# Kernel tuning notes

Measured on AMD Instinct MI355X. Metric: run time of the kernel, lower is better.

The kernel has to match this reference:

```python
import jax, jax.numpy as jnp
import numpy as np

B, T, D_IN, D_H, D_OUT = 64, 1024, 128, 512, 128


def setup_inputs() -> dict:
    key = jax.random.key(0)
    k1, k2, k3, k4, k5 = jax.random.split(key, 5)
    hscale = 0.1
    ifactor = 1.0 / np.sqrt(D_IN)
    hfactor = 1.0 / np.sqrt(D_H)
    pfactor = 1.0 / np.sqrt(D_H)
    return {
        "input_seq": jax.random.normal(k1, (B, T, D_IN), dtype=jnp.float32),
        "h0": jax.random.normal(k2, (D_H,), dtype=jnp.float32) * hscale,
        "wI": jax.random.normal(k3, (D_IN, D_H), dtype=jnp.float32) * ifactor,
        "wR": jax.random.normal(k4, (D_H, D_H), dtype=jnp.float32) * hfactor,
        "wO": jax.random.normal(k5, (D_H, D_OUT), dtype=jnp.float32) * pfactor,
    }


def reference(input_seq, h0, wI, wR, wO):
    # Precompute input projections for all timesteps at once: (B, T, D_H)
    xI = jnp.einsum("bti,ih->bth", input_seq, wI)
    h_init = jnp.broadcast_to(h0, (input_seq.shape[0], h0.shape[0]))

    def step(h, xI_t):
        h = jnp.tanh(xI_t + h @ wR)  # (B, D_H)
        return h, h

    # scan over time axis: move T to leading axis
    _, H = jax.lax.scan(step, h_init, jnp.swapaxes(xI, 0, 1))
    H = jnp.swapaxes(H, 0, 1)  # (B, T, D_H)
    O = jnp.einsum("bth,ho->bto", H, wO)  # (B, T, D_OUT)
    return O, H
```

## Files before the change

kernel.cpp:

```cpp
#include <hip/hip_runtime.h>
#include <cstdint>
#include <cstddef>

typedef _Float16 f16;
typedef _Float16 f16x4 __attribute__((ext_vector_type(4)));
typedef _Float16 f16x8 __attribute__((ext_vector_type(8)));
typedef float f32x4 __attribute__((ext_vector_type(4)));

#define MFMA16(a, b, c) __builtin_amdgcn_mfma_f32_16x16x16f16((a), (b), (c), 0, 0, 0)
#define MFMA32(a, b, c) __builtin_amdgcn_mfma_f32_16x16x32_f16((a), (b), (c), 0, 0, 0)

constexpr int TT = 1024, DIN = 128, DH = 512, DOUT = 128;
constexpr size_t O_ELEMS = (size_t)64 * 1024 * 128;

__device__ __forceinline__ uint32_t SW(uint32_t r) {
    return ((r & 7u) << 4) ^ ((r & 8u) << 2);
}

__global__ __launch_bounds__(256, 1) void k_xI(const float* __restrict__ X,
                                               const float* __restrict__ wI,
                                               float* __restrict__ xI) {
    __shared__ __align__(16) f16 Bt[DH][136];
    __shared__ __align__(16) f16 At[64][136];
    const int tid = threadIdx.x;
    const int wv = tid >> 6, ln = tid & 63, l15 = ln & 15, g = ln >> 4;
    const int m0 = (int)blockIdx.x * 64;

    #pragma unroll
    for (int u = 0; u < 16; ++u) {
        const int uid = u * 256 + tid;
        const int c4 = (uid & 127) << 2;
        const int r4 = (uid >> 7) << 2;
        float4 w[4];
        #pragma unroll
        for (int j = 0; j < 4; ++j)
            w[j] = *(const float4*)(wI + (size_t)(r4 + j) * DH + c4);
        #pragma unroll
        for (int n = 0; n < 4; ++n) {
            f16x4 v;
            #pragma unroll
            for (int j = 0; j < 4; ++j) v[j] = (f16)((&w[j].x)[n]);
            *(f16x4*)(&Bt[c4 + n][r4]) = v;
        }
    }
    {
        int r = tid >> 2;
        int cb = (tid & 3) << 5;
        #pragma unroll
        for (int u = 0; u < 8; ++u) {
            int c = cb + u * 4;
            const float4 x4 = *(const float4*)(X + (size_t)(m0 + r) * DIN + c);
            f16x4 h4;
            h4[0] = (f16)x4.x; h4[1] = (f16)x4.y; h4[2] = (f16)x4.z; h4[3] = (f16)x4.w;
            *(f16x4*)((char*)&At[r][0] + c * 2) = h4;
        }
    }
    __syncthreads();

    f32x4 acc[4][8];
    #pragma unroll
    for (int mt = 0; mt < 4; ++mt)
        #pragma unroll
        for (int nt = 0; nt < 8; ++nt) acc[mt][nt] = (f32x4){0.f, 0.f, 0.f, 0.f};

    #pragma unroll
    for (int c = 0; c < 8; ++c) {
        const int k0 = c * 16 + g * 4;
        f16x4 a[4];
        #pragma unroll
        for (int mt = 0; mt < 4; ++mt)
            a[mt] = *(const f16x4*)((const char*)&At[mt * 16 + l15][0] + k0 * 2);
        #pragma unroll
        for (int nt = 0; nt < 8; ++nt) {
            const int n = wv * 128 + nt * 16 + l15;
            const f16x4 b = *(const f16x4*)((const char*)&Bt[n][0] + k0 * 2);
            #pragma unroll
            for (int mt = 0; mt < 4; ++mt) acc[mt][nt] = MFMA16(a[mt], b, acc[mt][nt]);
        }
    }
    #pragma unroll
    for (int mt = 0; mt < 4; ++mt) {
        #pragma unroll
        for (int i = 0; i < 4; ++i) {
            const int m = m0 + mt * 16 + g * 4 + i;
            float* orow = xI + (size_t)m * DH + wv * 128 + l15;
            #pragma unroll
            for (int nt = 0; nt < 8; ++nt) orow[nt * 16] = acc[mt][nt][i];
        }
    }
}

__global__ __launch_bounds__(512, 2) void k_scan(const float* __restrict__ wR,
                                                 const float* __restrict__ h0,
                                                 float* __restrict__ Hb) {
    __shared__ __align__(16) char sm[163840];
    const int tid = threadIdx.x;
    const int wv = tid >> 6, ln = tid & 63, l15 = ln & 15, g = ln >> 4;
    const int bb = (int)blockIdx.x * 16;

    f16x8 Brf[3][16];
    #pragma unroll
    for (int q = 0; q < 3; ++q) {
        const int j = wv * 64 + q * 16 + l15;
        #pragma unroll
        for (int c = 0; c < 16; ++c) {
            const float* pw = wR + (size_t)(c * 32 + g * 8) * DH + j;
            f16x8 v;
            #pragma unroll
            for (int i = 0; i < 8; ++i) v[i] = (f16)pw[(size_t)i * DH];
            Brf[q][c] = v;
        }
    }
    for (int idx = tid; idx < 8 * 16 * 512; idx += 512) {
        const int j16 = idx & 15;
        const int k = (idx >> 4) & 511;
        const int t8 = idx >> 13;
        const float v = wR[(size_t)k * DH + t8 * 64 + 48 + j16];
        *(f16*)(sm + 32768 + t8 * 16384 + j16 * 1024 +
                (((uint32_t)(k * 2)) ^ SW((uint32_t)j16))) = (f16)v;
    }
    {
        const int j = tid;
        const f16 v = (f16)h0[j];
        #pragma unroll
        for (uint32_t r = 0; r < 16; ++r)
            *(f16*)(sm + r * 1024 + (((uint32_t)(j * 2)) ^ SW(r))) = v;
    }

    float* Hp = Hb + (size_t)(bb + l15) * TT * DH + wv * 64 + g * 4;

    const uint32_t pre =
        (((uint32_t)(g ^ (l15 & 7))) << 4) ^ (((uint32_t)(l15 & 8)) << 2);
    const uint32_t lanebase = (uint32_t)l15 * 1024;
    const uint32_t wbase = (uint32_t)(wv * 128 + g * 8);
    const uint32_t swl = SW((uint32_t)l15);

    f32x4 xr[4];
    #pragma unroll
    for (int q = 0; q < 4; ++q) xr[q] = *(const f32x4*)(Hp + q * 16);

    f32x4 acc[4];

    __syncthreads();

    #pragma unroll 1
    for (int t = 0; t < TT; ++t) {
        const uint32_t p = (uint32_t)(t & 1);
        #pragma unroll
        for (int q = 0; q < 4; ++q) acc[q] = xr[q];
        if (t + 1 < TT) {
            #pragma unroll
            for (int q = 0; q < 4; ++q) xr[q] = *(const f32x4*)(Hp + 512 + q * 16);
        }

        {
            const char* hbp = sm + p * 16384 + lanebase;
            const char* blp = sm + 32768 + (uint32_t)wv * 16384 + lanebase;
            f16x8 ab[3], b3[3];
            #pragma unroll
            for (int s = 0; s < 3; ++s) {
                const uint32_t off = (((uint32_t)s) << 6) ^ pre;
                ab[s] = *(const f16x8*)(hbp + off);
                b3[s] = *(const f16x8*)(blp + off);
            }
            #pragma unroll
            for (int c = 0; c < 16; ++c) {
                const int s = c % 3;
                const f16x8 a = ab[s];
                const f16x8 bt = b3[s];
                if (c < 13) {
                    const uint32_t off3 = (((uint32_t)(c + 3)) << 6) ^ pre;
                    ab[s] = *(const f16x8*)(hbp + off3);
                    b3[s] = *(const f16x8*)(blp + off3);
                }
                acc[0] = MFMA32(Brf[0][c], a, acc[0]);
                acc[1] = MFMA32(Brf[1][c], a, acc[1]);
                acc[2] = MFMA32(Brf[2][c], a, acc[2]);
                acc[3] = MFMA32(bt, a, acc[3]);
            }
        }

        {
            char* hw = sm + (p ^ 1u) * 16384 + lanebase;
            #pragma unroll
            for (int q = 0; q < 4; ++q) {
                f32x4 th4;
                f16x4 hv;
                #pragma unroll
                for (int i = 0; i < 4; ++i) {
                    const float x = acc[q][i];
                    const float e = __builtin_amdgcn_exp2f(x * 2.8853900817779268f);
                    const float th = 1.0f - 2.0f * __builtin_amdgcn_rcpf(e + 1.0f);
                    th4[i] = th;
                    hv[i] = (f16)th;
                }
                *(f32x4*)(Hp + q * 16) = th4;
                *(f16x4*)(hw + ((wbase + (uint32_t)q * 32) ^ swl)) = hv;
            }
        }
        asm volatile("s_waitcnt lgkmcnt(0)\n\ts_barrier" ::: "memory");

        Hp += DH;
    }
}

__global__ __launch_bounds__(256, 1) void k_O(const float* __restrict__ H,
                                              const float* __restrict__ wO,
                                              float* __restrict__ O) {
    __shared__ __align__(16) f16 Bt[DOUT][520];
    __shared__ __align__(16) f16 At[64][136];
    const int tid = threadIdx.x;
    const int wv = tid >> 6, ln = tid & 63, l15 = ln & 15, g = ln >> 4;
    const int m0 = (int)blockIdx.x * 64;

    #pragma unroll
    for (int u = 0; u < 16; ++u) {
        const int uid = u * 256 + tid;
        const int c4 = (uid & 31) << 2;
        const int r4 = (uid >> 5) << 2;
        float4 w[4];
        #pragma unroll
        for (int j = 0; j < 4; ++j)
            w[j] = *(const float4*)(wO + (size_t)(r4 + j) * DOUT + c4);
        #pragma unroll
        for (int n = 0; n < 4; ++n) {
            f16x4 v;
            #pragma unroll
            for (int j = 0; j < 4; ++j) v[j] = (f16)((&w[j].x)[n]);
            *(f16x4*)(&Bt[c4 + n][r4]) = v;
        }
    }

    f32x4 acc[8];
    #pragma unroll
    for (int nt = 0; nt < 8; ++nt) acc[nt] = (f32x4){0.f, 0.f, 0.f, 0.f};

    for (int kc = 0; kc < 4; ++kc) {
        __syncthreads();
        {
            int r = tid >> 2;
            int cb = (tid & 3) << 5;
            #pragma unroll
            for (int u = 0; u < 8; ++u) {
                int c = cb + u * 4;
                const float4 x4 = *(const float4*)(H + (size_t)(m0 + r) * DH + kc * 128 + c);
                f16x4 h4;
                h4[0] = (f16)x4.x; h4[1] = (f16)x4.y; h4[2] = (f16)x4.z; h4[3] = (f16)x4.w;
                *(f16x4*)((char*)&At[r][0] + c * 2) = h4;
            }
        }
        __syncthreads();
        #pragma unroll
        for (int c = 0; c < 8; ++c) {
            const int k0 = c * 16 + g * 4;
            const f16x4 a = *(const f16x4*)((const char*)&At[wv * 16 + l15][0] + k0 * 2);
            #pragma unroll
            for (int nt = 0; nt < 8; ++nt) {
                const f16x4 b =
                    *(const f16x4*)((const char*)&Bt[nt * 16 + l15][0] + (kc * 128 + k0) * 2);
                acc[nt] = MFMA16(a, b, acc[nt]);
            }
        }
    }
    #pragma unroll
    for (int i = 0; i < 4; ++i) {
        const int m = m0 + wv * 16 + g * 4 + i;
        #pragma unroll
        for (int nt = 0; nt < 8; ++nt) O[(size_t)m * DOUT + nt * 16 + l15] = acc[nt][i];
    }
}

extern "C" void kernel_launch(void* const* d_in, const int* in_sizes, int n_in,
                              void* d_out, int out_size, void* d_ws, size_t ws_size,
                              hipStream_t stream) {
    const float* X  = (const float*)d_in[0];
    const float* h0 = (const float*)d_in[1];
    const float* wI = (const float*)d_in[2];
    const float* wR = (const float*)d_in[3];
    const float* wO = (const float*)d_in[4];
    float* O = (float*)d_out;
    float* H = O + O_ELEMS;

    k_xI<<<1024, 256, 0, stream>>>(X, wI, H);
    k_scan<<<4, 512, 0, stream>>>(wR, h0, H);
    k_O<<<1024, 256, 0, stream>>>(H, wO, O);
}
```

Baseline: 2.104 ms.

## Rotate per-wave K-chunk order and prefetch own h slice before barrier

Each wave now walks the 16 K-chunks of the recurrent matmul starting at its own offset, and the register-held wR fragments are permuted to match. Because of that rotation, the first two h chunks a wave needs are the slice it just wrote itself. Those chunks, plus the first three LDS weight chunks, are loaded after lgkmcnt(0) but before s_barrier, so part of the LDS load latency is hidden behind the barrier wait. The aim is to shorten the serial per-timestep critical path, at the cost of more live registers and more complex address arithmetic.

```diff
diff --git a/kernel.cpp b/kernel.cpp
--- a/kernel.cpp
+++ b/kernel.cpp
@@ -104,7 +104,8 @@
         const int j = wv * 64 + q * 16 + l15;
         #pragma unroll
         for (int c = 0; c < 16; ++c) {
-            const float* pw = wR + (size_t)(c * 32 + g * 8) * DH + j;
+            const int kc = (2 * wv + c) & 15;
+            const float* pw = wR + (size_t)(kc * 32 + g * 8) * DH + j;
             f16x8 v;
             #pragma unroll
             for (int i = 0; i < 8; ++i) v[i] = (f16)pw[(size_t)i * DH];
@@ -129,6 +130,7 @@
 
     float* Hp = Hb + (size_t)(bb + l15) * TT * DH + wv * 64 + g * 4;
 
+    const uint32_t rb = ((uint32_t)wv) << 7;
     const uint32_t pre =
         (((uint32_t)(g ^ (l15 & 7))) << 4) ^ (((uint32_t)(l15 & 8)) << 2);
     const uint32_t lanebase = (uint32_t)l15 * 1024;
@@ -140,12 +142,31 @@
     for (int q = 0; q < 4; ++q) xr[q] = *(const f32x4*)(Hp + q * 16);
 
     f32x4 acc[4];
+    f16x8 ab[3], b3[3];
 
     __syncthreads();
+
+    {
+        const char* hbp = sm + lanebase;
+        const char* blp = sm + 32768 + (uint32_t)wv * 16384 + lanebase;
+        const uint32_t o0 = ((rb + 0u) & 960u) ^ pre;
+        const uint32_t o1 = ((rb + 64u) & 960u) ^ pre;
+        const uint32_t o2 = ((rb + 128u) & 960u) ^ pre;
+        ab[0] = *(const f16x8*)(hbp + o0);
+        ab[1] = *(const f16x8*)(hbp + o1);
+        b3[0] = *(const f16x8*)(blp + o0);
+        b3[1] = *(const f16x8*)(blp + o1);
+        b3[2] = *(const f16x8*)(blp + o2);
+    }
 
     #pragma unroll 1
     for (int t = 0; t < TT; ++t) {
         const uint32_t p = (uint32_t)(t & 1);
+        const char* hbp = sm + p * 16384 + lanebase;
+        const char* blp = sm + 32768 + (uint32_t)wv * 16384 + lanebase;
+
+        ab[2] = *(const f16x8*)(hbp + (((rb + 128u) & 960u) ^ pre));
+
         #pragma unroll
         for (int q = 0; q < 4; ++q) acc[q] = xr[q];
         if (t + 1 < TT) {
@@ -153,31 +174,20 @@
             for (int q = 0; q < 4; ++q) xr[q] = *(const f32x4*)(Hp + 512 + q * 16);
         }
 
-        {
-            const char* hbp = sm + p * 16384 + lanebase;
-            const char* blp = sm + 32768 + (uint32_t)wv * 16384 + lanebase;
-            f16x8 ab[3], b3[3];
-            #pragma unroll
-            for (int s = 0; s < 3; ++s) {
-                const uint32_t off = (((uint32_t)s) << 6) ^ pre;
-                ab[s] = *(const f16x8*)(hbp + off);
-                b3[s] = *(const f16x8*)(blp + off);
+        #pragma unroll
+        for (int c = 0; c < 16; ++c) {
+            const int s = c % 3;
+            const f16x8 a = ab[s];
+            const f16x8 bt = b3[s];
+            if (c < 13) {
+                const uint32_t off3 = ((rb + (uint32_t)((c + 3) << 6)) & 960u) ^ pre;
+                ab[s] = *(const f16x8*)(hbp + off3);
+                b3[s] = *(const f16x8*)(blp + off3);
             }
-            #pragma unroll
-            for (int c = 0; c < 16; ++c) {
-                const int s = c % 3;
-                const f16x8 a = ab[s];
-                const f16x8 bt = b3[s];
-                if (c < 13) {
-                    const uint32_t off3 = (((uint32_t)(c + 3)) << 6) ^ pre;
-                    ab[s] = *(const f16x8*)(hbp + off3);
-                    b3[s] = *(const f16x8*)(blp + off3);
-                }
-                acc[0] = MFMA32(Brf[0][c], a, acc[0]);
-                acc[1] = MFMA32(Brf[1][c], a, acc[1]);
-                acc[2] = MFMA32(Brf[2][c], a, acc[2]);
-                acc[3] = MFMA32(bt, a, acc[3]);
-            }
+            acc[0] = MFMA32(Brf[0][c], a, acc[0]);
+            acc[1] = MFMA32(Brf[1][c], a, acc[1]);
+            acc[2] = MFMA32(Brf[2][c], a, acc[2]);
+            acc[3] = MFMA32(bt, a, acc[3]);
         }
 
         {
@@ -198,7 +208,19 @@
                 *(f16x4*)(hw + ((wbase + (uint32_t)q * 32) ^ swl)) = hv;
             }
         }
-        asm volatile("s_waitcnt lgkmcnt(0)\n\ts_barrier" ::: "memory");
+        asm volatile("s_waitcnt lgkmcnt(0)" ::: "memory");
+        {
+            const char* hbn = sm + (p ^ 1u) * 16384 + lanebase;
+            const uint32_t o0 = ((rb + 0u) & 960u) ^ pre;
+            const uint32_t o1 = ((rb + 64u) & 960u) ^ pre;
+            const uint32_t o2 = ((rb + 128u) & 960u) ^ pre;
+            ab[0] = *(const f16x8*)(hbn + o0);
+            ab[1] = *(const f16x8*)(hbn + o1);
+            b3[0] = *(const f16x8*)(blp + o0);
+            b3[1] = *(const f16x8*)(blp + o1);
+            b3[2] = *(const f16x8*)(blp + o2);
+        }
+        asm volatile("s_barrier" ::: "memory");
 
         Hp += DH;
     }
```

After: 3.843 ms. 82.7% more time.
